# Kernel optimization log

Measured on AMD Instinct MI355X. Metric: run time of the kernel, lower is better.

Reference implementation:

```python
import jax, jax.numpy as jnp
import numpy as np

HIDDEN_DIM = 2048
NUM_HEADS = 16
HEAD_DIM = HIDDEN_DIM // NUM_HEADS


def setup_inputs() -> dict:
    key = jax.random.key(0)
    ks = jax.random.split(key, 5)
    B, S, D = 2, 2048, HIDDEN_DIM
    scale = 1.0 / np.sqrt(D)
    return {
        "x": jax.random.normal(ks[0], (B, S, D), dtype=jnp.float32),
        "w_q": jax.random.normal(ks[1], (D, D), dtype=jnp.float32) * scale,
        "w_k": jax.random.normal(ks[2], (D, D), dtype=jnp.float32) * scale,
        "w_v": jax.random.normal(ks[3], (D, D), dtype=jnp.float32) * scale,
        "w_o": jax.random.normal(ks[4], (D, D), dtype=jnp.float32) * scale,
        "causal": 1,
    }


def _attention(q, k, v, causal):
    # q,k,v: (B, S, D) -> split heads -> (B, H, S, d)
    B, S, D = q.shape
    q = q.reshape(B, S, NUM_HEADS, HEAD_DIM).transpose(0, 2, 1, 3)
    k = k.reshape(B, S, NUM_HEADS, HEAD_DIM).transpose(0, 2, 1, 3)
    v = v.reshape(B, S, NUM_HEADS, HEAD_DIM).transpose(0, 2, 1, 3)
    scale = 1.0 / np.sqrt(HEAD_DIM)
    # scores: (B, H, S, S)
    s = jnp.einsum("bhqd,bhkd->bhqk", q, k) * scale
    if causal:
        qpos = jnp.arange(S)[:, None]
        kpos = jnp.arange(S)[None, :]
        s = jnp.where(kpos > qpos, -jnp.inf, s)
    # stable softmax; rows that are fully -inf cannot occur with causal mask
    p = jax.nn.softmax(s, axis=-1)
    o = jnp.einsum("bhqk,bhkd->bhqd", p, v)
    return o.transpose(0, 2, 1, 3).reshape(B, S, D)


def reference(x, w_q, w_k, w_v, w_o, causal):
    q = x @ w_q.T
    k = x @ w_k.T
    v = x @ w_v.T
    o = _attention(q, k, v, bool(causal))
    return o @ w_o.T
```

## Files before the change

kernel.cpp:

```cpp
#include <hip/hip_runtime.h>


typedef __attribute__((ext_vector_type(8))) short short8;
typedef __attribute__((ext_vector_type(4))) short bfs4;
typedef __attribute__((ext_vector_type(4))) float floatx4;

__device__ __forceinline__ void gl_lds16(const void* g, void* l) {
  __builtin_amdgcn_global_load_lds((const __attribute__((address_space(1))) void*)g,
                                   (__attribute__((address_space(3))) void*)l, 16, 0, 0);
}

__device__ __forceinline__ short f2bf(float f) {
  union { float f; unsigned u; } a; a.f = f;
  unsigned r = a.u + 0x7FFFu + ((a.u >> 16) & 1u);
  return (short)(r >> 16);
}

__global__ __launch_bounds__(256) void cvt_bf16(
    const float* __restrict__ s0, const float* __restrict__ s1,
    const float* __restrict__ s2, const float* __restrict__ s3,
    const float* __restrict__ s4,
    short* __restrict__ d0, short* __restrict__ d1, short* __restrict__ d2,
    short* __restrict__ d3, short* __restrict__ d4,
    int n0, int nw) {
  const int z = blockIdx.z;
  const float* s = (z == 0) ? s0 : (z == 1) ? s1 : (z == 2) ? s2 : (z == 3) ? s3 : s4;
  short* d      = (z == 0) ? d0 : (z == 1) ? d1 : (z == 2) ? d2 : (z == 3) ? d3 : d4;
  const int n   = (z == 0) ? n0 : nw;
  const int stride = gridDim.x * blockDim.x * 4;
  for (int i = (blockIdx.x * blockDim.x + threadIdx.x) * 4; i < n; i += stride) {
    float4 v = *(const float4*)(s + i);
    bfs4 o;
    o[0] = f2bf(v.x); o[1] = f2bf(v.y); o[2] = f2bf(v.z); o[3] = f2bf(v.w);
    *(bfs4*)(d + i) = o;
  }
}

__global__ __launch_bounds__(256, 2) void gemm_bt(
    const short* __restrict__ A,
    const short* __restrict__ B0, const short* __restrict__ B1, const short* __restrict__ B2,
    short* __restrict__ C0, short* __restrict__ C1, short* __restrict__ C2,
    int M, int N, int K) {
  const short* Bm = (blockIdx.z == 0) ? B0 : ((blockIdx.z == 1) ? B1 : B2);
  short* C = (blockIdx.z == 0) ? C0 : ((blockIdx.z == 1) ? C1 : C2);

  __shared__ short As[128 * 64];
  __shared__ short Bs[128 * 64];

  const int tid = threadIdx.x;
  const int w = tid >> 6, l = tid & 63;
  const int lane15 = l & 15, quad = l >> 4;
  const int wr = w >> 1, wc = w & 1;
  const int row0 = blockIdx.y * 128;
  const int col0 = blockIdx.x * 128;

  floatx4 acc[4][4] = {};
  const int srow = l >> 3;
  const int sg = l & 7;

  for (int k0 = 0; k0 < K; k0 += 64) {
#pragma unroll
    for (int j = 0; j < 4; ++j) {
      int chunk = j * 4 + w;
      int row = chunk * 8 + srow;
      int g = sg ^ (row & 7);
      gl_lds16(A  + (size_t)(row0 + row) * K + k0 + g * 8, &As[chunk * 512]);
      gl_lds16(Bm + (size_t)(col0 + row) * K + k0 + g * 8, &Bs[chunk * 512]);
    }
    __syncthreads();
#pragma unroll
    for (int ks = 0; ks < 2; ++ks) {
      short8 af[4], bf[4];
#pragma unroll
      for (int i = 0; i < 4; ++i) {
        int rowA = wr * 64 + i * 16 + lane15;
        af[i] = *(const short8*)&As[rowA * 64 + (((ks * 4 + quad) ^ (rowA & 7)) << 3)];
        int rowB = wc * 64 + i * 16 + lane15;
        bf[i] = *(const short8*)&Bs[rowB * 64 + (((ks * 4 + quad) ^ (rowB & 7)) << 3)];
      }
#pragma unroll
      for (int i = 0; i < 4; ++i)
#pragma unroll
        for (int jj = 0; jj < 4; ++jj)
          acc[i][jj] = __builtin_amdgcn_mfma_f32_16x16x32_bf16(af[i], bf[jj], acc[i][jj], 0, 0, 0);
    }
    __syncthreads();
  }

#pragma unroll
  for (int i = 0; i < 4; ++i)
#pragma unroll
    for (int jj = 0; jj < 4; ++jj)
#pragma unroll
      for (int r = 0; r < 4; ++r) {
        int row = row0 + wr * 64 + i * 16 + quad * 4 + r;
        int col = col0 + wc * 64 + jj * 16 + lane15;
        C[(size_t)row * N + col] = f2bf(acc[i][jj][r]);
      }
}

__global__ __launch_bounds__(256, 2) void gemm_bt_f32out(
    const short* __restrict__ A, const short* __restrict__ Bm,
    float* __restrict__ C, int M, int N, int K) {
  __shared__ short As[128 * 64];
  __shared__ short Bs[128 * 64];

  const int tid = threadIdx.x;
  const int w = tid >> 6, l = tid & 63;
  const int lane15 = l & 15, quad = l >> 4;
  const int wr = w >> 1, wc = w & 1;
  const int row0 = blockIdx.y * 128;
  const int col0 = blockIdx.x * 128;

  floatx4 acc[4][4] = {};
  const int srow = l >> 3;
  const int sg = l & 7;

  for (int k0 = 0; k0 < K; k0 += 64) {
#pragma unroll
    for (int j = 0; j < 4; ++j) {
      int chunk = j * 4 + w;
      int row = chunk * 8 + srow;
      int g = sg ^ (row & 7);
      gl_lds16(A  + (size_t)(row0 + row) * K + k0 + g * 8, &As[chunk * 512]);
      gl_lds16(Bm + (size_t)(col0 + row) * K + k0 + g * 8, &Bs[chunk * 512]);
    }
    __syncthreads();
#pragma unroll
    for (int ks = 0; ks < 2; ++ks) {
      short8 af[4], bf[4];
#pragma unroll
      for (int i = 0; i < 4; ++i) {
        int rowA = wr * 64 + i * 16 + lane15;
        af[i] = *(const short8*)&As[rowA * 64 + (((ks * 4 + quad) ^ (rowA & 7)) << 3)];
        int rowB = wc * 64 + i * 16 + lane15;
        bf[i] = *(const short8*)&Bs[rowB * 64 + (((ks * 4 + quad) ^ (rowB & 7)) << 3)];
      }
#pragma unroll
      for (int i = 0; i < 4; ++i)
#pragma unroll
        for (int jj = 0; jj < 4; ++jj)
          acc[i][jj] = __builtin_amdgcn_mfma_f32_16x16x32_bf16(af[i], bf[jj], acc[i][jj], 0, 0, 0);
    }
    __syncthreads();
  }

#pragma unroll
  for (int i = 0; i < 4; ++i)
#pragma unroll
    for (int jj = 0; jj < 4; ++jj)
#pragma unroll
      for (int r = 0; r < 4; ++r) {
        int row = row0 + wr * 64 + i * 16 + quad * 4 + r;
        int col = col0 + wc * 64 + jj * 16 + lane15;
        C[(size_t)row * N + col] = acc[i][jj][r];
      }
}

__global__ __launch_bounds__(512, 4) void attn_fused(
    const short* __restrict__ Qg, const short* __restrict__ Kg,
    const short* __restrict__ Vg, short* __restrict__ Og,
    const int* __restrict__ causal_p) {
  constexpr int S = 2048, D = 2048, HDim = 128;
  constexpr int PS = 40;
  __shared__ __align__(16) short smem[38144];
  short* Ps  = smem + 32768;
  float* aLds = (float*)(smem + 37888);
  short* Qs  = smem;
  floatx4* F4 = (floatx4*)smem;

  const int tid = threadIdx.x;
  const int w = tid >> 6, l = tid & 63;
  const int lane15 = l & 15, quad = l >> 4;
  const int w4 = w & 3, grp = w >> 2;
  const int nlin = blockIdx.y * 16 + blockIdx.x;
  const int pairx = (nlin >> 3) & 15;
  const int bh = (nlin & 7) * 4 + (nlin >> 7);
  const int b = bh >> 4, h = bh & 15;
  const size_t rbase = (size_t)b * S;
  const int c0 = h * HDim;
  const int causal = *causal_p;
  short* Pw = Ps + w * (16 * PS);
  constexpr float SCL = 0.08838834764831845f * 1.4426950408889634f;

  const int krow = w * 4 + quad;
  const int kgs = lane15 ^ (krow & 7);
  const int vrow = l >> 1;
  const int vcol = w * 16 + (l & 1) * 8;

#pragma unroll 1
  for (int ph = 0; ph < 2; ++ph) {
    const int jt = ph ? (31 - pairx) : pairx;
    const int q0 = jt * 64;
    const int wrow0 = q0 + w4 * 16;

#pragma unroll
    for (int j = 0; j < 2; ++j) {
      int row = j * 32 + w * 4 + quad;
      int gs = lane15 ^ (row & 7);
      gl_lds16(Qg + (rbase + q0 + row) * D + c0 + gs * 8, &Qs[(j * 8 + w) * 512]);
    }
    __syncthreads();
    short8 qf[4];
#pragma unroll
    for (int ks = 0; ks < 4; ++ks) {
      int row = w4 * 16 + lane15;
      qf[ks] = *(const short8*)&Qs[row * HDim + (((ks * 4 + quad) ^ (row & 7)) << 3)];
    }
    __syncthreads();

    floatx4 ot[8] = {};
    float psum[4] = {0.f, 0.f, 0.f, 0.f};
    const int ktiles = causal ? (q0 / 32 + 2) : (S / 32);
    const int iters = ktiles >> 1;

    short* Kcur = smem;
    short* Knxt = smem + 8192;
    short* Vcur = smem + 16384;
    short* Vnxt = smem + 24576;

    gl_lds16(Kg + (rbase + krow) * D + c0 + kgs * 8, &Kcur[w * 512]);
    gl_lds16(Kg + (rbase + 32 + krow) * D + c0 + kgs * 8, &Kcur[4096 + w * 512]);
    gl_lds16(Vg + (rbase + vrow) * D + c0 + vcol, &Vcur[w * 512]);
    gl_lds16(Vg + (rbase + 32 + vrow) * D + c0 + vcol, &Vcur[4096 + w * 512]);
    __syncthreads();

    for (int it = 0; it < iters; ++it) {
      const int k0A = it * 64;
      const bool pf = (it + 1 < iters);
      if (pf) {
        const int k0N = k0A + 64;
        gl_lds16(Kg + (rbase + k0N + krow) * D + c0 + kgs * 8, &Knxt[w * 512]);
        gl_lds16(Kg + (rbase + k0N + 32 + krow) * D + c0 + kgs * 8, &Knxt[4096 + w * 512]);
        gl_lds16(Vg + (rbase + k0N + vrow) * D + c0 + vcol, &Vnxt[w * 512]);
        gl_lds16(Vg + (rbase + k0N + 32 + vrow) * D + c0 + vcol, &Vnxt[4096 + w * 512]);
      }

      const int k0 = k0A + grp * 32;
      const short* Kc = Kcur + grp * 4096;
      const short* Vc = Vcur + grp * 4096;
      if (!causal || k0 <= wrow0 + 15) {
        const bool diag = causal && (k0 + 32 > wrow0);
        floatx4 sacc[2] = {};
        __builtin_amdgcn_s_setprio(1);
#pragma unroll
        for (int ks = 0; ks < 4; ++ks) {
          short8 kf0, kf1;
          {
            int row = lane15;
            kf0 = *(const short8*)&Kc[row * HDim + (((ks * 4 + quad) ^ (row & 7)) << 3)];
            row = 16 + lane15;
            kf1 = *(const short8*)&Kc[row * HDim + (((ks * 4 + quad) ^ (row & 7)) << 3)];
          }
          sacc[0] = __builtin_amdgcn_mfma_f32_16x16x32_bf16(qf[ks], kf0, sacc[0], 0, 0, 0);
          sacc[1] = __builtin_amdgcn_mfma_f32_16x16x32_bf16(qf[ks], kf1, sacc[1], 0, 0, 0);
        }
        __builtin_amdgcn_s_setprio(0);
#pragma unroll
        for (int r = 0; r < 4; ++r) {
          int prow = quad * 4 + r;
          float s0 = fminf(sacc[0][r] * SCL, 115.0f);
          float s1 = fminf(sacc[1][r] * SCL, 115.0f);
          float p0 = exp2f(s0);
          float p1 = exp2f(s1);
          if (diag) {
            int qrow = wrow0 + prow;
            if (k0 + lane15 > qrow)      p0 = 0.f;
            if (k0 + 16 + lane15 > qrow) p1 = 0.f;
          }
          psum[r] += p0 + p1;
          unsigned pk;
          asm("v_cvt_pk_bf16_f32 %0, %1, %2" : "=v"(pk) : "v"(p0), "v"(p1));
          Pw[prow * PS + lane15]      = (short)pk;
          Pw[prow * PS + 16 + lane15] = (short)(pk >> 16);
        }
        short8 pfr = *(const short8*)&Pw[lane15 * PS + quad * 8];
        const unsigned vbase = (unsigned)(size_t)Vc + (quad << 8) + (lane15 << 3);
        bfs4 vlo[8], vhi[8];
#pragma unroll
        for (int cd = 0; cd < 8; ++cd)
          asm volatile("ds_read_b64_tr_b16 %0, %2\n\t"
                       "ds_read_b64_tr_b16 %1, %2 offset:128"
                       : "=&v"(vlo[cd]), "=&v"(vhi[cd])
                       : "v"(vbase + (cd << 10)));
        asm volatile("s_waitcnt lgkmcnt(0)" ::: "memory");
        __builtin_amdgcn_sched_barrier(0);
        __builtin_amdgcn_s_setprio(1);
#pragma unroll
        for (int cd = 0; cd < 8; ++cd) {
          short8 vf = {vlo[cd][0], vlo[cd][1], vlo[cd][2], vlo[cd][3],
                       vhi[cd][0], vhi[cd][1], vhi[cd][2], vhi[cd][3]};
          ot[cd] = __builtin_amdgcn_mfma_f32_16x16x32_bf16(vf, pfr, ot[cd], 0, 0, 0);
        }
        __builtin_amdgcn_s_setprio(0);
      }

      __syncthreads();
      short* t = Kcur; Kcur = Knxt; Knxt = t;
      t = Vcur; Vcur = Vnxt; Vnxt = t;
    }

#pragma unroll
    for (int r = 0; r < 4; ++r) {
      float s = psum[r];
      s += __shfl_xor(s, 1, 64);
      s += __shfl_xor(s, 2, 64);
      s += __shfl_xor(s, 4, 64);
      s += __shfl_xor(s, 8, 64);
      if (lane15 == 0) aLds[grp * 64 + w4 * 16 + quad * 4 + r] = s;
    }
    if (grp == 1) {
      int qrow = w4 * 16 + lane15;
#pragma unroll
      for (int cd = 0; cd < 8; ++cd)
        F4[qrow * 32 + ((cd * 4 + quad) ^ ((qrow & 7) << 2))] = ot[cd];
    }
    __syncthreads();
    float invq = 0.f;
    if (grp == 0) {
      int qrow = w4 * 16 + lane15;
      invq = 1.0f / (aLds[qrow] + aLds[64 + qrow]);
#pragma unroll
      for (int cd = 0; cd < 8; ++cd) {
        floatx4 o2 = F4[qrow * 32 + ((cd * 4 + quad) ^ ((qrow & 7) << 2))];
        ot[cd] += o2;
      }
    }
    __syncthreads();
    if (grp == 0) {
      int qrow = w4 * 16 + lane15;
#pragma unroll
      for (int cd = 0; cd < 8; ++cd)
#pragma unroll
        for (int r = 0; r < 4; ++r) {
          int col = cd * 16 + quad * 4 + r;
          Qs[qrow * HDim + (((col >> 3) ^ (qrow & 7)) << 3) + (col & 7)] =
              f2bf(ot[cd][r] * invq);
        }
    }
    __syncthreads();
#pragma unroll
    for (int i = 0; i < 2; ++i) {
      int c = i * 512 + tid;
      int row = c >> 4, g = c & 15;
      *(short8*)(Og + (rbase + q0 + row) * D + c0 + g * 8) =
          *(const short8*)&Qs[row * HDim + ((g ^ (row & 7)) << 3)];
    }
    __syncthreads();
  }
}

extern "C" void kernel_launch(void* const* d_in, const int* in_sizes, int n_in,
                              void* d_out, int out_size, void* d_ws, size_t ws_size,
                              hipStream_t stream) {
  const float* x  = (const float*)d_in[0];
  const float* wq = (const float*)d_in[1];
  const float* wk = (const float*)d_in[2];
  const float* wv = (const float*)d_in[3];
  const float* wo = (const float*)d_in[4];
  const int* causal = (const int*)d_in[5];
  float* out = (float*)d_out;

  const int M = 4096, N = 2048, K = 2048;
  const int NX = M * K;
  const int NW = N * K;

  char* ws = (char*)d_ws;
  short* xb  = (short*)(ws);
  short* wqb = (short*)(ws + 16u * 1024 * 1024);
  short* wkb = (short*)(ws + 24u * 1024 * 1024);
  short* wvb = (short*)(ws + 32u * 1024 * 1024);
  short* wob = (short*)(ws + 40u * 1024 * 1024);
  short* q   = (short*)(ws + 48u * 1024 * 1024);
  short* k   = (short*)(ws + 64u * 1024 * 1024);
  short* v   = (short*)(ws + 80u * 1024 * 1024);
  short* o   = (short*)(ws + 96u * 1024 * 1024);

  dim3 blk(256);
  cvt_bf16<<<dim3(2048, 1, 5), blk, 0, stream>>>(x, wq, wk, wv, wo,
                                                 xb, wqb, wkb, wvb, wob, NX, NW);
  gemm_bt<<<dim3(N / 128, M / 128, 3), blk, 0, stream>>>(xb, wqb, wkb, wvb,
                                                         q, k, v, M, N, K);
  attn_fused<<<dim3(16, 32), dim3(512), 0, stream>>>(q, k, v, o, causal);
  gemm_bt_f32out<<<dim3(N / 128, M / 128, 1), blk, 0, stream>>>(o, wob, out, M, N, K);
}
```

Measured before the change: 370.3 us.

## Halve attention block to 4 waves, each wave computing 32 query rows

The attention kernel now runs with 256 threads instead of 512. Each wave handles two 16-row query subtiles and reuses every K fragment and V transposed read for both, which halves LDS reads per MFMA. Each wave now issues four staging loads per tile instead of two. The cost is more accumulator registers per wave (two sets of output tiles), fewer waves per block to hide latency, and a causal skip check per 16-row subtile.

```diff
diff --git a/kernel.cpp b/kernel.cpp
--- a/kernel.cpp
+++ b/kernel.cpp
@@ -157,22 +157,22 @@
       }
 }
 
-__global__ __launch_bounds__(512, 4) void attn_fused(
+__global__ __launch_bounds__(256, 2) void attn_fused(
     const short* __restrict__ Qg, const short* __restrict__ Kg,
     const short* __restrict__ Vg, short* __restrict__ Og,
     const int* __restrict__ causal_p) {
   constexpr int S = 2048, D = 2048, HDim = 128;
   constexpr int PS = 40;
-  __shared__ __align__(16) short smem[38144];
+  __shared__ __align__(16) short smem[35584];
   short* Ps  = smem + 32768;
-  float* aLds = (float*)(smem + 37888);
+  float* aLds = (float*)(smem + 35328);
   short* Qs  = smem;
   floatx4* F4 = (floatx4*)smem;
 
   const int tid = threadIdx.x;
   const int w = tid >> 6, l = tid & 63;
   const int lane15 = l & 15, quad = l >> 4;
-  const int w4 = w & 3, grp = w >> 2;
+  const int wk = w & 1, grp = w >> 1;
   const int nlin = blockIdx.y * 16 + blockIdx.x;
   const int pairx = (nlin >> 3) & 15;
   const int bh = (nlin & 7) * 4 + (nlin >> 7);
@@ -183,34 +183,51 @@
   short* Pw = Ps + w * (16 * PS);
   constexpr float SCL = 0.08838834764831845f * 1.4426950408889634f;
 
-  const int krow = w * 4 + quad;
-  const int kgs = lane15 ^ (krow & 7);
-  const int vrow = l >> 1;
-  const int vcol = w * 16 + (l & 1) * 8;
+  const int vs = l >> 1;
+  const int vdo = (l & 1) * 8;
+
+#define STAGE_KV(Kb, Vb, kbase)                                                \
+  {                                                                            \
+    _Pragma("unroll") for (int j = 0; j < 4; ++j) {                            \
+      int idx = w * 4 + j; int t = idx >> 3; int ch = idx & 7;                 \
+      int row = ch * 4 + quad; int g = lane15 ^ (row & 7);                     \
+      gl_lds16(Kg + (rbase + (kbase) + t * 32 + row) * D + c0 + g * 8,         \
+               &(Kb)[t * 4096 + ch * 512]);                                    \
+    }                                                                          \
+    _Pragma("unroll") for (int j = 0; j < 4; ++j) {                            \
+      int idx = w * 4 + j; int t = idx >> 3; int db = idx & 7;                 \
+      gl_lds16(Vg + (rbase + (kbase) + t * 32 + vs) * D + c0 + db * 16 + vdo,  \
+               &(Vb)[t * 4096 + db * 512]);                                    \
+    }                                                                          \
+  }
 
 #pragma unroll 1
   for (int ph = 0; ph < 2; ++ph) {
     const int jt = ph ? (31 - pairx) : pairx;
     const int q0 = jt * 64;
-    const int wrow0 = q0 + w4 * 16;
-
-#pragma unroll
-    for (int j = 0; j < 2; ++j) {
-      int row = j * 32 + w * 4 + quad;
+    const int qrow0 = q0 + wk * 32;
+
+#pragma unroll
+    for (int j = 0; j < 4; ++j) {
+      int chunk = j * 4 + w;
+      int row = chunk * 4 + quad;
       int gs = lane15 ^ (row & 7);
-      gl_lds16(Qg + (rbase + q0 + row) * D + c0 + gs * 8, &Qs[(j * 8 + w) * 512]);
-    }
-    __syncthreads();
-    short8 qf[4];
-#pragma unroll
-    for (int ks = 0; ks < 4; ++ks) {
-      int row = w4 * 16 + lane15;
-      qf[ks] = *(const short8*)&Qs[row * HDim + (((ks * 4 + quad) ^ (row & 7)) << 3)];
-    }
-    __syncthreads();
-
-    floatx4 ot[8] = {};
-    float psum[4] = {0.f, 0.f, 0.f, 0.f};
+      gl_lds16(Qg + (rbase + q0 + row) * D + c0 + gs * 8, &Qs[chunk * 512]);
+    }
+    __syncthreads();
+    short8 qf[2][4];
+#pragma unroll
+    for (int rs = 0; rs < 2; ++rs)
+#pragma unroll
+      for (int ks = 0; ks < 4; ++ks) {
+        int row = wk * 32 + rs * 16 + lane15;
+        qf[rs][ks] = *(const short8*)&Qs[row * HDim + (((ks * 4 + quad) ^ (row & 7)) << 3)];
+      }
+    __syncthreads();
+
+    floatx4 ot0[8] = {}, ot1[8] = {};
+    float psum0[4] = {0.f, 0.f, 0.f, 0.f};
+    float psum1[4] = {0.f, 0.f, 0.f, 0.f};
     const int ktiles = causal ? (q0 / 32 + 2) : (S / 32);
     const int iters = ktiles >> 1;
 
@@ -219,29 +236,20 @@
     short* Vcur = smem + 16384;
     short* Vnxt = smem + 24576;
 
-    gl_lds16(Kg + (rbase + krow) * D + c0 + kgs * 8, &Kcur[w * 512]);
-    gl_lds16(Kg + (rbase + 32 + krow) * D + c0 + kgs * 8, &Kcur[4096 + w * 512]);
-    gl_lds16(Vg + (rbase + vrow) * D + c0 + vcol, &Vcur[w * 512]);
-    gl_lds16(Vg + (rbase + 32 + vrow) * D + c0 + vcol, &Vcur[4096 + w * 512]);
+    STAGE_KV(Kcur, Vcur, 0)
     __syncthreads();
 
     for (int it = 0; it < iters; ++it) {
       const int k0A = it * 64;
-      const bool pf = (it + 1 < iters);
-      if (pf) {
-        const int k0N = k0A + 64;
-        gl_lds16(Kg + (rbase + k0N + krow) * D + c0 + kgs * 8, &Knxt[w * 512]);
-        gl_lds16(Kg + (rbase + k0N + 32 + krow) * D + c0 + kgs * 8, &Knxt[4096 + w * 512]);
-        gl_lds16(Vg + (rbase + k0N + vrow) * D + c0 + vcol, &Vnxt[w * 512]);
-        gl_lds16(Vg + (rbase + k0N + 32 + vrow) * D + c0 + vcol, &Vnxt[4096 + w * 512]);
-      }
+      if (it + 1 < iters) STAGE_KV(Knxt, Vnxt, k0A + 64)
 
       const int k0 = k0A + grp * 32;
       const short* Kc = Kcur + grp * 4096;
       const short* Vc = Vcur + grp * 4096;
-      if (!causal || k0 <= wrow0 + 15) {
-        const bool diag = causal && (k0 + 32 > wrow0);
-        floatx4 sacc[2] = {};
+      const bool act1 = !causal || k0 <= qrow0 + 31;
+      const bool act0 = !causal || k0 <= qrow0 + 15;
+      if (act1) {
+        floatx4 sacc0[2] = {}, sacc1[2] = {};
         __builtin_amdgcn_s_setprio(1);
 #pragma unroll
         for (int ks = 0; ks < 4; ++ks) {
@@ -252,47 +260,85 @@
             row = 16 + lane15;
             kf1 = *(const short8*)&Kc[row * HDim + (((ks * 4 + quad) ^ (row & 7)) << 3)];
           }
-          sacc[0] = __builtin_amdgcn_mfma_f32_16x16x32_bf16(qf[ks], kf0, sacc[0], 0, 0, 0);
-          sacc[1] = __builtin_amdgcn_mfma_f32_16x16x32_bf16(qf[ks], kf1, sacc[1], 0, 0, 0);
+          sacc1[0] = __builtin_amdgcn_mfma_f32_16x16x32_bf16(qf[1][ks], kf0, sacc1[0], 0, 0, 0);
+          sacc1[1] = __builtin_amdgcn_mfma_f32_16x16x32_bf16(qf[1][ks], kf1, sacc1[1], 0, 0, 0);
+          if (act0) {
+            sacc0[0] = __builtin_amdgcn_mfma_f32_16x16x32_bf16(qf[0][ks], kf0, sacc0[0], 0, 0, 0);
+            sacc0[1] = __builtin_amdgcn_mfma_f32_16x16x32_bf16(qf[0][ks], kf1, sacc0[1], 0, 0, 0);
+          }
         }
         __builtin_amdgcn_s_setprio(0);
-#pragma unroll
-        for (int r = 0; r < 4; ++r) {
-          int prow = quad * 4 + r;
-          float s0 = fminf(sacc[0][r] * SCL, 115.0f);
-          float s1 = fminf(sacc[1][r] * SCL, 115.0f);
-          float p0 = exp2f(s0);
-          float p1 = exp2f(s1);
-          if (diag) {
-            int qrow = wrow0 + prow;
-            if (k0 + lane15 > qrow)      p0 = 0.f;
-            if (k0 + 16 + lane15 > qrow) p1 = 0.f;
+
+        short8 pfr0, pfr1;
+        {
+          const bool diag = causal && (k0 + 32 > qrow0 + 16);
+#pragma unroll
+          for (int r = 0; r < 4; ++r) {
+            int prow = quad * 4 + r;
+            float s0 = fminf(sacc1[0][r] * SCL, 115.0f);
+            float s1 = fminf(sacc1[1][r] * SCL, 115.0f);
+            float p0 = exp2f(s0);
+            float p1 = exp2f(s1);
+            if (diag) {
+              int qrow = qrow0 + 16 + prow;
+              if (k0 + lane15 > qrow)      p0 = 0.f;
+              if (k0 + 16 + lane15 > qrow) p1 = 0.f;
+            }
+            psum1[r] += p0 + p1;
+            unsigned pk;
+            asm("v_cvt_pk_bf16_f32 %0, %1, %2" : "=v"(pk) : "v"(p0), "v"(p1));
+            Pw[prow * PS + lane15]      = (short)pk;
+            Pw[prow * PS + 16 + lane15] = (short)(pk >> 16);
           }
-          psum[r] += p0 + p1;
-          unsigned pk;
-          asm("v_cvt_pk_bf16_f32 %0, %1, %2" : "=v"(pk) : "v"(p0), "v"(p1));
-          Pw[prow * PS + lane15]      = (short)pk;
-          Pw[prow * PS + 16 + lane15] = (short)(pk >> 16);
+          pfr1 = *(const short8*)&Pw[lane15 * PS + quad * 8];
         }
-        short8 pfr = *(const short8*)&Pw[lane15 * PS + quad * 8];
+        if (act0) {
+          const bool diag = causal && (k0 + 32 > qrow0);
+#pragma unroll
+          for (int r = 0; r < 4; ++r) {
+            int prow = quad * 4 + r;
+            float s0 = fminf(sacc0[0][r] * SCL, 115.0f);
+            float s1 = fminf(sacc0[1][r] * SCL, 115.0f);
+            float p0 = exp2f(s0);
+            float p1 = exp2f(s1);
+            if (diag) {
+              int qrow = qrow0 + prow;
+              if (k0 + lane15 > qrow)      p0 = 0.f;
+              if (k0 + 16 + lane15 > qrow) p1 = 0.f;
+            }
+            psum0[r] += p0 + p1;
+            unsigned pk;
+            asm("v_cvt_pk_bf16_f32 %0, %1, %2" : "=v"(pk) : "v"(p0), "v"(p1));
+            Pw[prow * PS + lane15]      = (short)pk;
+            Pw[prow * PS + 16 + lane15] = (short)(pk >> 16);
+          }
+          pfr0 = *(const short8*)&Pw[lane15 * PS + quad * 8];
+        }
+
         const unsigned vbase = (unsigned)(size_t)Vc + (quad << 8) + (lane15 << 3);
-        bfs4 vlo[8], vhi[8];
-#pragma unroll
-        for (int cd = 0; cd < 8; ++cd)
-          asm volatile("ds_read_b64_tr_b16 %0, %2\n\t"
-                       "ds_read_b64_tr_b16 %1, %2 offset:128"
-                       : "=&v"(vlo[cd]), "=&v"(vhi[cd])
-                       : "v"(vbase + (cd << 10)));
-        asm volatile("s_waitcnt lgkmcnt(0)" ::: "memory");
-        __builtin_amdgcn_sched_barrier(0);
-        __builtin_amdgcn_s_setprio(1);
-#pragma unroll
-        for (int cd = 0; cd < 8; ++cd) {
-          short8 vf = {vlo[cd][0], vlo[cd][1], vlo[cd][2], vlo[cd][3],
-                       vhi[cd][0], vhi[cd][1], vhi[cd][2], vhi[cd][3]};
-          ot[cd] = __builtin_amdgcn_mfma_f32_16x16x32_bf16(vf, pfr, ot[cd], 0, 0, 0);
+#pragma unroll
+        for (int cg = 0; cg < 2; ++cg) {
+          bfs4 vlo[4], vhi[4];
+#pragma unroll
+          for (int j = 0; j < 4; ++j)
+            asm volatile("ds_read_b64_tr_b16 %0, %2\n\t"
+                         "ds_read_b64_tr_b16 %1, %2 offset:128"
+                         : "=&v"(vlo[j]), "=&v"(vhi[j])
+                         : "v"(vbase + ((cg * 4 + j) << 10)));
+          asm volatile("s_waitcnt lgkmcnt(0)" ::: "memory");
+          __builtin_amdgcn_sched_barrier(0);
+          __builtin_amdgcn_s_setprio(1);
+#pragma unroll
+          for (int j = 0; j < 4; ++j) {
+            int cd = cg * 4 + j;
+            short8 vf = {vlo[j][0], vlo[j][1], vlo[j][2], vlo[j][3],
+                         vhi[j][0], vhi[j][1], vhi[j][2], vhi[j][3]};
+            ot1[cd] = __builtin_amdgcn_mfma_f32_16x16x32_bf16(vf, pfr1, ot1[cd], 0, 0, 0);
+            if (act0)
+              ot0[cd] = __builtin_amdgcn_mfma_f32_16x16x32_bf16(vf, pfr0, ot0[cd], 0, 0, 0);
+          }
+          __builtin_amdgcn_s_setprio(0);
         }
-        __builtin_amdgcn_s_setprio(0);
       }
 
       __syncthreads();
@@ -301,53 +347,64 @@
     }
 
 #pragma unroll
-    for (int r = 0; r < 4; ++r) {
-      float s = psum[r];
-      s += __shfl_xor(s, 1, 64);
-      s += __shfl_xor(s, 2, 64);
-      s += __shfl_xor(s, 4, 64);
-      s += __shfl_xor(s, 8, 64);
-      if (lane15 == 0) aLds[grp * 64 + w4 * 16 + quad * 4 + r] = s;
-    }
+    for (int rs = 0; rs < 2; ++rs)
+#pragma unroll
+      for (int r = 0; r < 4; ++r) {
+        float s = rs ? psum1[r] : psum0[r];
+        s += __shfl_xor(s, 1, 64);
+        s += __shfl_xor(s, 2, 64);
+        s += __shfl_xor(s, 4, 64);
+        s += __shfl_xor(s, 8, 64);
+        if (lane15 == 0) aLds[grp * 64 + wk * 32 + rs * 16 + quad * 4 + r] = s;
+      }
     if (grp == 1) {
-      int qrow = w4 * 16 + lane15;
-#pragma unroll
-      for (int cd = 0; cd < 8; ++cd)
-        F4[qrow * 32 + ((cd * 4 + quad) ^ ((qrow & 7) << 2))] = ot[cd];
-    }
-    __syncthreads();
-    float invq = 0.f;
+#pragma unroll
+      for (int cd = 0; cd < 8; ++cd) {
+        int q0r = wk * 32 + lane15;
+        F4[q0r * 32 + ((cd * 4 + quad) ^ ((q0r & 7) << 2))] = ot0[cd];
+        int q1r = wk * 32 + 16 + lane15;
+        F4[q1r * 32 + ((cd * 4 + quad) ^ ((q1r & 7) << 2))] = ot1[cd];
+      }
+    }
+    __syncthreads();
+    float invq0 = 0.f, invq1 = 0.f;
     if (grp == 0) {
-      int qrow = w4 * 16 + lane15;
-      invq = 1.0f / (aLds[qrow] + aLds[64 + qrow]);
+      int q0r = wk * 32 + lane15;
+      int q1r = wk * 32 + 16 + lane15;
+      invq0 = 1.0f / (aLds[q0r] + aLds[64 + q0r]);
+      invq1 = 1.0f / (aLds[q1r] + aLds[64 + q1r]);
 #pragma unroll
       for (int cd = 0; cd < 8; ++cd) {
-        floatx4 o2 = F4[qrow * 32 + ((cd * 4 + quad) ^ ((qrow & 7) << 2))];
-        ot[cd] += o2;
+        ot0[cd] += F4[q0r * 32 + ((cd * 4 + quad) ^ ((q0r & 7) << 2))];
+        ot1[cd] += F4[q1r * 32 + ((cd * 4 + quad) ^ ((q1r & 7) << 2))];
       }
     }
     __syncthreads();
     if (grp == 0) {
-      int qrow = w4 * 16 + lane15;
 #pragma unroll
       for (int cd = 0; cd < 8; ++cd)
 #pragma unroll
         for (int r = 0; r < 4; ++r) {
           int col = cd * 16 + quad * 4 + r;
-          Qs[qrow * HDim + (((col >> 3) ^ (qrow & 7)) << 3) + (col & 7)] =
-              f2bf(ot[cd][r] * invq);
+          int q0r = wk * 32 + lane15;
+          Qs[q0r * HDim + (((col >> 3) ^ (q0r & 7)) << 3) + (col & 7)] =
+              f2bf(ot0[cd][r] * invq0);
+          int q1r = wk * 32 + 16 + lane15;
+          Qs[q1r * HDim + (((col >> 3) ^ (q1r & 7)) << 3) + (col & 7)] =
+              f2bf(ot1[cd][r] * invq1);
         }
     }
     __syncthreads();
 #pragma unroll
-    for (int i = 0; i < 2; ++i) {
-      int c = i * 512 + tid;
+    for (int i = 0; i < 4; ++i) {
+      int c = i * 256 + tid;
       int row = c >> 4, g = c & 15;
       *(short8*)(Og + (rbase + q0 + row) * D + c0 + g * 8) =
           *(const short8*)&Qs[row * HDim + ((g ^ (row & 7)) << 3)];
     }
     __syncthreads();
   }
+#undef STAGE_KV
 }
 
 extern "C" void kernel_launch(void* const* d_in, const int* in_sizes, int n_in,
@@ -381,6 +438,6 @@
                                                  xb, wqb, wkb, wvb, wob, NX, NW);
   gemm_bt<<<dim3(N / 128, M / 128, 3), blk, 0, stream>>>(xb, wqb, wkb, wvb,
                                                          q, k, v, M, N, K);
-  attn_fused<<<dim3(16, 32), dim3(512), 0, stream>>>(q, k, v, o, causal);
+  attn_fused<<<dim3(16, 32), blk, 0, stream>>>(q, k, v, o, causal);
   gemm_bt_f32out<<<dim3(N / 128, M / 128, 1), blk, 0, stream>>>(o, wob, out, M, N, K);
 }
```

Result: no change. 363.5 us (median of 2 runs) (-1.8%).
